# Kernel optimization log

Measured on AMD Instinct MI355X. Metric: run time of the kernel, lower is better.

## Reference

```python
import jax, jax.numpy as jnp
import numpy as np

N_NODES = 100000
N_EDGES = 1600000
HIDDEN = 128
LEAKY_SLOPE = 0.01  # torch F.leaky_relu default


def setup_inputs() -> dict:
    key = jax.random.key(0)
    k1, k2, k3, k4 = jax.random.split(key, 4)
    x = jax.random.normal(k1, (N_NODES, HIDDEN), dtype=jnp.float32)
    edge_index = jax.random.randint(k2, (2, N_EDGES), 0, N_NODES, dtype=jnp.int64)
    # nn.Linear(hidden, 1, bias=False) weights, stored as [hidden] vectors
    w_i = jax.random.normal(k3, (HIDDEN,), dtype=jnp.float32) * (1.0 / np.sqrt(HIDDEN))
    w_j = jax.random.normal(k4, (HIDDEN,), dtype=jnp.float32) * (1.0 / np.sqrt(HIDDEN))
    return {"x": x, "edge_index": edge_index, "w_i": w_i, "w_j": w_j}


def _segment_softmax(e, seg, num_segments):
    # numerically stable softmax over variable-length groups keyed by seg
    seg_max = jax.ops.segment_max(e, seg, num_segments=num_segments)
    seg_max = jnp.where(jnp.isfinite(seg_max), seg_max, 0.0)  # empty segments
    e_exp = jnp.exp(e - seg_max[seg])
    denom = jax.ops.segment_sum(e_exp, seg, num_segments=num_segments)
    return e_exp / denom[seg]


def reference(x, edge_index, w_i, w_j):
    n = x.shape[0]
    idx_j = edge_index[0]  # edge_index_j (softmax groups)
    idx_i = edge_index[1]  # edge_index_i (aggregation destinations)
    # per-node attention logits, gathered per edge
    ei_all = x @ w_i  # [N]
    ej_all = x @ w_j  # [N]
    e = ei_all[idx_i] + ej_all[idx_j]  # [E]
    e = jnp.where(e > 0, e, LEAKY_SLOPE * e)  # leaky_relu
    alpha = _segment_softmax(e.astype(jnp.float32), idx_j, n)  # [E]
    # spmm(edge_index[[1,0]], alpha, N, N, x): out[idx_i] += alpha * x[idx_j]
    msgs = alpha[:, None] * x[idx_j]  # [E, hidden]
    out = jax.ops.segment_sum(msgs, idx_i, num_segments=n)
    return jax.nn.relu(out)
```

## Files before the change

kernel.cpp:

```cpp
#include <hip/hip_runtime.h>

#define N_HID 128
#define LEAKY 0.01f
#define EPB   4096
#define SCB   1024

__device__ inline ushort f2bf_rne(float f) {
    unsigned u = __float_as_uint(f);
    u += 0x7fffu + ((u >> 16) & 1u);
    return (ushort)(u >> 16);
}

__device__ inline int load_idx(const void* eidx, long long pos, int is64) {
    if (is64) return (int)((const long long*)eidx)[pos];
    return ((const int*)eidx)[pos];
}

__global__ void detect_dtype_k(const void* __restrict__ eidx, long long n_i64,
                               int* __restrict__ flag) {
    __shared__ int nonzero_hi;
    if (threadIdx.x == 0) nonzero_hi = 0;
    __syncthreads();
    const long long* p = (const long long*)eidx;
    long long samples = n_i64 < 4096 ? n_i64 : 4096;
    int bad = 0;
    for (long long k = threadIdx.x; k < samples; k += blockDim.x) {
        if ((p[k] >> 32) != 0) bad = 1;
    }
    if (bad) atomicOr(&nonzero_hi, 1);
    __syncthreads();
    if (threadIdx.x == 0) *flag = nonzero_hi ? 0 : 1;
}

__global__ __launch_bounds__(256) void node_logits_k(
        const float* __restrict__ x, const float* __restrict__ w_i,
        const float* __restrict__ w_j, float* __restrict__ ei_all,
        float* __restrict__ ej_all, ushort* __restrict__ xb, int n) {
    int wave = (int)((blockIdx.x * (long long)blockDim.x + threadIdx.x) >> 6);
    int lane = threadIdx.x & 63;
    if (wave >= n) return;
    const float2* xr = (const float2*)(x + (long long)wave * N_HID);
    float2 v  = xr[lane];
    float2 wi = ((const float2*)w_i)[lane];
    float2 wj = ((const float2*)w_j)[lane];
    if (xb) {
        unsigned packed = (unsigned)f2bf_rne(v.x) | ((unsigned)f2bf_rne(v.y) << 16);
        ((unsigned*)(xb + (long long)wave * N_HID))[lane] = packed;
    }
    float si = v.x * wi.x + v.y * wi.y;
    float sj = v.x * wj.x + v.y * wj.y;
    #pragma unroll
    for (int off = 32; off >= 1; off >>= 1) {
        si += __shfl_xor(si, off);
        sj += __shfl_xor(sj, off);
    }
    if (lane == 0) {
        ei_all[wave] = si;
        ej_all[wave] = sj;
    }
}

__global__ __launch_bounds__(256) void hist_k(
        const void* __restrict__ eidx, const int* __restrict__ flag,
        unsigned* __restrict__ tabI, unsigned* __restrict__ tabJ,
        long long E, int nblkA, int NB) {
    __shared__ unsigned hi[512], hj[512];
    for (int b = threadIdx.x; b < NB; b += 256) { hi[b] = 0; hj[b] = 0; }
    __syncthreads();
    int is64 = *flag;
    long long k0 = (long long)blockIdx.x * EPB;
    #pragma unroll 4
    for (int m = 0; m < EPB / 256; ++m) {
        long long k = k0 + m * 256 + threadIdx.x;
        if (k < E) {
            int j = load_idx(eidx, k, is64);
            int i = load_idx(eidx, E + k, is64);
            atomicAdd(&hi[i >> 8], 1u);
            atomicAdd(&hj[j >> 8], 1u);
        }
    }
    __syncthreads();
    for (int b = threadIdx.x; b < NB; b += 256) {
        tabI[(size_t)b * nblkA + blockIdx.x] = hi[b];
        tabJ[(size_t)b * nblkA + blockIdx.x] = hj[b];
    }
}

__global__ __launch_bounds__(SCB) void scanT1_k(unsigned* __restrict__ a,
                                                unsigned* __restrict__ bs, int nt) {
    __shared__ unsigned tmp[SCB];
    int gid = blockIdx.x * SCB + threadIdx.x;
    unsigned v = (gid < nt) ? a[gid] : 0;
    tmp[threadIdx.x] = v;
    __syncthreads();
    for (int off = 1; off < SCB; off <<= 1) {
        unsigned t = (threadIdx.x >= off) ? tmp[threadIdx.x - off] : 0;
        __syncthreads();
        tmp[threadIdx.x] += t;
        __syncthreads();
    }
    if (gid < nt) a[gid] = tmp[threadIdx.x] - v;
    if (threadIdx.x == SCB - 1) bs[blockIdx.x] = tmp[threadIdx.x];
}

__global__ __launch_bounds__(SCB) void scanT2_k(unsigned* __restrict__ bs, int nb) {
    __shared__ unsigned tmp[SCB];
    unsigned v = (threadIdx.x < nb) ? bs[threadIdx.x] : 0;
    tmp[threadIdx.x] = v;
    __syncthreads();
    for (int off = 1; off < SCB; off <<= 1) {
        unsigned t = (threadIdx.x >= off) ? tmp[threadIdx.x - off] : 0;
        __syncthreads();
        tmp[threadIdx.x] += t;
        __syncthreads();
    }
    if (threadIdx.x < nb) bs[threadIdx.x] = tmp[threadIdx.x] - v;
}

__global__ __launch_bounds__(SCB) void scanT3_k(unsigned* __restrict__ a,
                                                const unsigned* __restrict__ bs,
                                                int nt) {
    int gid = blockIdx.x * SCB + threadIdx.x;
    if (gid < nt) a[gid] += bs[gid / SCB];
}

__global__ __launch_bounds__(256) void scatter2_k(
        const void* __restrict__ eidx, const int* __restrict__ flag,
        const unsigned* __restrict__ tabI, const unsigned* __restrict__ tabJ,
        unsigned* __restrict__ srecI, unsigned* __restrict__ srecJ,
        long long E, int nblkA, int NB) {
    __shared__ unsigned ci[512], cj[512];
    unsigned Eu = (unsigned)E;
    for (int b = threadIdx.x; b < NB; b += 256) {
        ci[b] = tabI[(size_t)b * nblkA + blockIdx.x];
        cj[b] = tabJ[(size_t)b * nblkA + blockIdx.x] - Eu;
    }
    __syncthreads();
    int is64 = *flag;
    long long k0 = (long long)blockIdx.x * EPB;
    #pragma unroll 4
    for (int m = 0; m < EPB / 256; ++m) {
        long long k = k0 + m * 256 + threadIdx.x;
        if (k < E) {
            int j = load_idx(eidx, k, is64);
            int i = load_idx(eidx, E + k, is64);
            unsigned pI = atomicAdd(&ci[i >> 8], 1u);
            srecI[pI] = ((unsigned)(i & 255) << 17) | (unsigned)j;
            unsigned pJ = atomicAdd(&cj[j >> 8], 1u);
            srecJ[pJ] = ((unsigned)(j & 255) << 17) | (unsigned)i;
        }
    }
}

__global__ __launch_bounds__(256) void finalizeJ_k(
        const unsigned* __restrict__ srecJ, const unsigned* __restrict__ tabJ,
        const float* __restrict__ ei_all, const float* __restrict__ ej_all,
        float* __restrict__ denom, int n, long long E, int nblkA, int NB) {
    int b = blockIdx.x;
    int tid = threadIdx.x;
    unsigned Eu = (unsigned)E;
    int base = (int)(tabJ[(size_t)b * nblkA] - Eu);
    int end  = (b + 1 < NB) ? (int)(tabJ[(size_t)(b + 1) * nblkA] - Eu) : (int)E;

    __shared__ float ejl[256];
    __shared__ float dsum[256];
    int g = b * 256 + tid;
    ejl[tid]  = (g < n) ? ej_all[g] : 0.f;
    dsum[tid] = 0.f;
    __syncthreads();

    for (int t = base + tid; t < end; t += 256) {
        unsigned r = srecJ[t];
        int jl = (int)(r >> 17);
        int i  = (int)(r & 0x1FFFFu);
        float e = ei_all[i] + ejl[jl];
        e = e > 0.f ? e : LEAKY * e;
        atomicAdd(&dsum[jl], __expf(e));
    }
    __syncthreads();
    if (g < n) denom[g] = dsum[tid];
}

__global__ __launch_bounds__(256) void finalizeI_k(
        const unsigned* __restrict__ srecI, const unsigned* __restrict__ tabI,
        const float* __restrict__ ei_all, const float* __restrict__ ej_all,
        const float* __restrict__ denom, int* __restrict__ start,
        unsigned* __restrict__ pje, int n, long long E, int nblkA, int NB) {
    int b = blockIdx.x;
    int tid = threadIdx.x;
    int base = (int)tabI[(size_t)b * nblkA];
    int end  = (b + 1 < NB) ? (int)tabI[(size_t)(b + 1) * nblkA] : (int)E;

    __shared__ int cnt[256];
    __shared__ int off[256];
    __shared__ float eil[256];
    int g = b * 256 + tid;
    cnt[tid] = 0;
    eil[tid] = (g < n) ? ei_all[g] : 0.f;
    __syncthreads();

    for (int t = base + tid; t < end; t += 256)
        atomicAdd(&cnt[srecI[t] >> 17], 1);
    __syncthreads();

    int v = cnt[tid];
    off[tid] = v;
    __syncthreads();
    for (int s = 1; s < 256; s <<= 1) {
        int t2 = (tid >= s) ? off[tid - s] : 0;
        __syncthreads();
        off[tid] += t2;
        __syncthreads();
    }
    int excl = off[tid] - v;
    if (g < n) start[g] = base + excl;
    if (b == NB - 1 && tid == 0) start[n] = (int)E;

    cnt[tid] = excl;
    __syncthreads();

    for (int t = base + tid; t < end; t += 256) {
        unsigned r = srecI[t];
        int il = (int)(r >> 17);
        int j  = (int)(r & 0x1FFFFu);
        float e = eil[il] + ej_all[j];
        e = e > 0.f ? e : LEAKY * e;
        float alpha = __expf(e) / denom[j];
        unsigned aq = __float2uint_rn(alpha * 32768.f);
        if (aq > 32767u) aq = 32767u;
        int slot = base + atomicAdd(&cnt[il], 1);
        pje[slot] = ((unsigned)j << 15) | aq;
    }
}

__global__ __launch_bounds__(256) void gather_bf16_k(
        const int* __restrict__ start, const unsigned* __restrict__ pje,
        const ushort* __restrict__ xb, float* __restrict__ out, int n) {
    int wave = (int)((blockIdx.x * (long long)blockDim.x + threadIdx.x) >> 6);
    int lane = threadIdx.x & 63;
    if (wave >= n) return;
    int s = start[wave];
    int e_end = start[wave + 1];
    int sub = lane >> 4;
    int col = lane & 15;

    float a0 = 0.f, a1 = 0.f, a2 = 0.f, a3 = 0.f;
    float a4 = 0.f, a5 = 0.f, a6 = 0.f, a7 = 0.f;
    for (int e = s; e < e_end; e += 8) {
        int ee0 = e + sub;
        int ee1 = e + 4 + sub;
        unsigned cur0 = (ee0 < e_end) ? pje[ee0] : 0u;
        unsigned cur1 = (ee1 < e_end) ? pje[ee1] : 0u;
        float af0 = (float)(cur0 & 0x7FFFu) * (1.f / 32768.f);
        float af1 = (float)(cur1 & 0x7FFFu) * (1.f / 32768.f);
        uint4 u0 = ((const uint4*)(xb + (size_t)(cur0 >> 15) * N_HID))[col];
        uint4 u1 = ((const uint4*)(xb + (size_t)(cur1 >> 15) * N_HID))[col];
        a0 += af0 * __uint_as_float(u0.x << 16);
        a1 += af0 * __uint_as_float(u0.x & 0xffff0000u);
        a2 += af0 * __uint_as_float(u0.y << 16);
        a3 += af0 * __uint_as_float(u0.y & 0xffff0000u);
        a4 += af0 * __uint_as_float(u0.z << 16);
        a5 += af0 * __uint_as_float(u0.z & 0xffff0000u);
        a6 += af0 * __uint_as_float(u0.w << 16);
        a7 += af0 * __uint_as_float(u0.w & 0xffff0000u);
        a0 += af1 * __uint_as_float(u1.x << 16);
        a1 += af1 * __uint_as_float(u1.x & 0xffff0000u);
        a2 += af1 * __uint_as_float(u1.y << 16);
        a3 += af1 * __uint_as_float(u1.y & 0xffff0000u);
        a4 += af1 * __uint_as_float(u1.z << 16);
        a5 += af1 * __uint_as_float(u1.z & 0xffff0000u);
        a6 += af1 * __uint_as_float(u1.w << 16);
        a7 += af1 * __uint_as_float(u1.w & 0xffff0000u);
    }
    a0 += __shfl_xor(a0, 16); a1 += __shfl_xor(a1, 16);
    a2 += __shfl_xor(a2, 16); a3 += __shfl_xor(a3, 16);
    a4 += __shfl_xor(a4, 16); a5 += __shfl_xor(a5, 16);
    a6 += __shfl_xor(a6, 16); a7 += __shfl_xor(a7, 16);
    a0 += __shfl_xor(a0, 32); a1 += __shfl_xor(a1, 32);
    a2 += __shfl_xor(a2, 32); a3 += __shfl_xor(a3, 32);
    a4 += __shfl_xor(a4, 32); a5 += __shfl_xor(a5, 32);
    a6 += __shfl_xor(a6, 32); a7 += __shfl_xor(a7, 32);

    float4* orow = (float4*)(out + (size_t)wave * N_HID);
    if (sub == 0) {
        float4 r;
        r.x = fmaxf(a0, 0.f); r.y = fmaxf(a1, 0.f);
        r.z = fmaxf(a2, 0.f); r.w = fmaxf(a3, 0.f);
        orow[col * 2] = r;
    } else if (sub == 1) {
        float4 r;
        r.x = fmaxf(a4, 0.f); r.y = fmaxf(a5, 0.f);
        r.z = fmaxf(a6, 0.f); r.w = fmaxf(a7, 0.f);
        orow[col * 2 + 1] = r;
    }
}

__global__ __launch_bounds__(256) void gather_f32_k(
        const int* __restrict__ start, const unsigned* __restrict__ pje,
        const float* __restrict__ x, float* __restrict__ out, int n) {
    int wave = (int)((blockIdx.x * (long long)blockDim.x + threadIdx.x) >> 6);
    int lane = threadIdx.x & 63;
    if (wave >= n) return;
    int s = start[wave];
    int e_end = start[wave + 1];
    float ax = 0.f, ay = 0.f;
    unsigned ja = 0;
    if (s < e_end) ja = pje[s];
    for (int e = s; e < e_end; ++e) {
        unsigned cur = ja;
        if (e + 1 < e_end) ja = pje[e + 1];
        float a = (float)(cur & 0x7FFFu) * (1.f / 32768.f);
        float2 v = ((const float2*)(x + (long long)(cur >> 15) * N_HID))[lane];
        ax += a * v.x;
        ay += a * v.y;
    }
    float2 r;
    r.x = fmaxf(ax, 0.f);
    r.y = fmaxf(ay, 0.f);
    ((float2*)(out + (long long)wave * N_HID))[lane] = r;
}

extern "C" void kernel_launch(void* const* d_in, const int* in_sizes, int n_in,
                              void* d_out, int out_size, void* d_ws,
                              size_t ws_size, hipStream_t stream) {
    const float* x   = (const float*)d_in[0];
    const void*  eix = d_in[1];
    const float* w_i = (const float*)d_in[2];
    const float* w_j = (const float*)d_in[3];
    float* out = (float*)d_out;

    int n = in_sizes[0] / N_HID;
    long long E = in_sizes[1] / 2;

    int nblkA = (int)((E + EPB - 1) / EPB);
    int NB    = (n + 255) / 256;
    int NT    = NB * nblkA;
    int NT2   = 2 * NT;
    int nb1   = (NT2 + SCB - 1) / SCB;

    char* p = (char*)d_ws;
    float* ei_all = (float*)p;               p += (size_t)n * 4;
    float* ej_all = (float*)p;               p += (size_t)n * 4;
    float* denom  = (float*)p;               p += (size_t)n * 4;
    int*   start  = (int*)p;                 p += ((size_t)(n + 1) * 4 + 15) & ~15ull;
    unsigned* tab = (unsigned*)p;            p += ((size_t)NT2 * 4 + 15) & ~15ull;
    unsigned* tabI = tab;
    unsigned* tabJ = tab + NT;
    unsigned* bs1 = (unsigned*)p;            p += (size_t)SCB * 4;
    int*   flag   = (int*)p;                 p += 16;
    unsigned* srecI = (unsigned*)p;          p += (size_t)E * 4;
    unsigned* pje   = (unsigned*)p;          p += (size_t)E * 4;
    unsigned* srecJ = pje;
    ushort* xb    = (ushort*)p;              p += (size_t)n * N_HID * 2;
    int wsBig = ((size_t)(p - (char*)d_ws) <= ws_size);
    if (!wsBig) xb = nullptr;

    detect_dtype_k<<<1, 256, 0, stream>>>(eix, E * 2, flag);

    long long t1 = (long long)n * 64;
    node_logits_k<<<(unsigned)((t1 + 255) / 256), 256, 0, stream>>>(
        x, w_i, w_j, ei_all, ej_all, xb, n);

    hist_k<<<nblkA, 256, 0, stream>>>(eix, flag, tabI, tabJ, E, nblkA, NB);

    scanT1_k<<<nb1, SCB, 0, stream>>>(tab, bs1, NT2);
    scanT2_k<<<1, SCB, 0, stream>>>(bs1, nb1);
    scanT3_k<<<nb1, SCB, 0, stream>>>(tab, bs1, NT2);

    scatter2_k<<<nblkA, 256, 0, stream>>>(eix, flag, tabI, tabJ, srecI, srecJ,
                                          E, nblkA, NB);

    finalizeJ_k<<<NB, 256, 0, stream>>>(srecJ, tabJ, ei_all, ej_all, denom,
                                        n, E, nblkA, NB);

    finalizeI_k<<<NB, 256, 0, stream>>>(srecI, tabI, ei_all, ej_all, denom,
                                        start, pje, n, E, nblkA, NB);

    long long t4 = (long long)n * 64;
    if (wsBig) {
        gather_bf16_k<<<(unsigned)((t4 + 255) / 256), 256, 0, stream>>>(
            start, pje, xb, out, n);
    } else {
        gather_f32_k<<<(unsigned)((t4 + 255) / 256), 256, 0, stream>>>(
            start, pje, x, out, n);
    }
}
```

Before: 202.9 us.

## Fold scan block offsets into consumers, widen finalize blocks, pack logit/denominator

Drops the third scan pass by having scatter and both finalize kernels add the per-chunk scan offset on the fly when reading the table. The finalize kernels now launch with 512 threads over each 256-node bucket to expose more parallelism. The j-side logit and softmax denominator are packed into one float2 so the I-side gather does one load per edge. EPB is also halved, which doubles the number of histogram blocks and the size of the prefix table.

```diff
diff --git a/kernel.cpp b/kernel.cpp
--- a/kernel.cpp
+++ b/kernel.cpp
@@ -2,8 +2,9 @@
 
 #define N_HID 128
 #define LEAKY 0.01f
-#define EPB   4096
+#define EPB   2048
 #define SCB   1024
+#define TABV(g) (tab[g] + bs1[(g) >> 10])
 
 __device__ inline ushort f2bf_rne(float f) {
     unsigned u = __float_as_uint(f);
@@ -117,23 +118,18 @@
     if (threadIdx.x < nb) bs[threadIdx.x] = tmp[threadIdx.x] - v;
 }
 
-__global__ __launch_bounds__(SCB) void scanT3_k(unsigned* __restrict__ a,
-                                                const unsigned* __restrict__ bs,
-                                                int nt) {
-    int gid = blockIdx.x * SCB + threadIdx.x;
-    if (gid < nt) a[gid] += bs[gid / SCB];
-}
-
 __global__ __launch_bounds__(256) void scatter2_k(
         const void* __restrict__ eidx, const int* __restrict__ flag,
-        const unsigned* __restrict__ tabI, const unsigned* __restrict__ tabJ,
+        const unsigned* __restrict__ tab, const unsigned* __restrict__ bs1,
         unsigned* __restrict__ srecI, unsigned* __restrict__ srecJ,
-        long long E, int nblkA, int NB) {
+        long long E, int nblkA, int NB, int NT) {
     __shared__ unsigned ci[512], cj[512];
     unsigned Eu = (unsigned)E;
     for (int b = threadIdx.x; b < NB; b += 256) {
-        ci[b] = tabI[(size_t)b * nblkA + blockIdx.x];
-        cj[b] = tabJ[(size_t)b * nblkA + blockIdx.x] - Eu;
+        size_t gI = (size_t)b * nblkA + blockIdx.x;
+        size_t gJ = (size_t)NT + gI;
+        ci[b] = TABV(gI);
+        cj[b] = TABV(gJ) - Eu;
     }
     __syncthreads();
     int is64 = *flag;
@@ -152,24 +148,28 @@
     }
 }
 
-__global__ __launch_bounds__(256) void finalizeJ_k(
-        const unsigned* __restrict__ srecJ, const unsigned* __restrict__ tabJ,
-        const float* __restrict__ ei_all, const float* __restrict__ ej_all,
-        float* __restrict__ denom, int n, long long E, int nblkA, int NB) {
+__global__ __launch_bounds__(512) void finalizeJ_k(
+        const unsigned* __restrict__ srecJ, const unsigned* __restrict__ tab,
+        const unsigned* __restrict__ bs1, const float* __restrict__ ei_all,
+        const float* __restrict__ ej_all, float2* __restrict__ ejd,
+        int n, long long E, int nblkA, int NB, int NT) {
     int b = blockIdx.x;
     int tid = threadIdx.x;
     unsigned Eu = (unsigned)E;
-    int base = (int)(tabJ[(size_t)b * nblkA] - Eu);
-    int end  = (b + 1 < NB) ? (int)(tabJ[(size_t)(b + 1) * nblkA] - Eu) : (int)E;
+    size_t gJ0 = (size_t)NT + (size_t)b * nblkA;
+    int base = (int)(TABV(gJ0) - Eu);
+    int end  = (b + 1 < NB) ? (int)(TABV(gJ0 + nblkA) - Eu) : (int)E;
 
     __shared__ float ejl[256];
     __shared__ float dsum[256];
     int g = b * 256 + tid;
-    ejl[tid]  = (g < n) ? ej_all[g] : 0.f;
-    dsum[tid] = 0.f;
-    __syncthreads();
-
-    for (int t = base + tid; t < end; t += 256) {
+    if (tid < 256) {
+        ejl[tid]  = (g < n) ? ej_all[g] : 0.f;
+        dsum[tid] = 0.f;
+    }
+    __syncthreads();
+
+    for (int t = base + tid; t < end; t += 512) {
         unsigned r = srecJ[t];
         int jl = (int)(r >> 17);
         int i  = (int)(r & 0x1FFFFu);
@@ -178,54 +178,66 @@
         atomicAdd(&dsum[jl], __expf(e));
     }
     __syncthreads();
-    if (g < n) denom[g] = dsum[tid];
-}
-
-__global__ __launch_bounds__(256) void finalizeI_k(
-        const unsigned* __restrict__ srecI, const unsigned* __restrict__ tabI,
-        const float* __restrict__ ei_all, const float* __restrict__ ej_all,
-        const float* __restrict__ denom, int* __restrict__ start,
-        unsigned* __restrict__ pje, int n, long long E, int nblkA, int NB) {
+    if (tid < 256 && g < n) {
+        float2 r2;
+        r2.x = ejl[tid];
+        r2.y = dsum[tid];
+        ejd[g] = r2;
+    }
+}
+
+__global__ __launch_bounds__(512) void finalizeI_k(
+        const unsigned* __restrict__ srecI, const unsigned* __restrict__ tab,
+        const unsigned* __restrict__ bs1, const float* __restrict__ ei_all,
+        const float2* __restrict__ ejd, int* __restrict__ start,
+        unsigned* __restrict__ pje, int n, long long E, int nblkA, int NB,
+        int NT) {
     int b = blockIdx.x;
     int tid = threadIdx.x;
-    int base = (int)tabI[(size_t)b * nblkA];
-    int end  = (b + 1 < NB) ? (int)tabI[(size_t)(b + 1) * nblkA] : (int)E;
+    size_t gI0 = (size_t)b * nblkA;
+    int base = (int)TABV(gI0);
+    int end  = (b + 1 < NB) ? (int)TABV(gI0 + nblkA) : (int)E;
 
     __shared__ int cnt[256];
     __shared__ int off[256];
     __shared__ float eil[256];
     int g = b * 256 + tid;
-    cnt[tid] = 0;
-    eil[tid] = (g < n) ? ei_all[g] : 0.f;
-    __syncthreads();
-
-    for (int t = base + tid; t < end; t += 256)
+    if (tid < 256) {
+        cnt[tid] = 0;
+        eil[tid] = (g < n) ? ei_all[g] : 0.f;
+    }
+    __syncthreads();
+
+    for (int t = base + tid; t < end; t += 512)
         atomicAdd(&cnt[srecI[t] >> 17], 1);
     __syncthreads();
 
-    int v = cnt[tid];
-    off[tid] = v;
+    int v = 0;
+    if (tid < 256) { v = cnt[tid]; off[tid] = v; }
     __syncthreads();
     for (int s = 1; s < 256; s <<= 1) {
-        int t2 = (tid >= s) ? off[tid - s] : 0;
-        __syncthreads();
-        off[tid] += t2;
-        __syncthreads();
-    }
-    int excl = off[tid] - v;
-    if (g < n) start[g] = base + excl;
+        int t2 = 0;
+        if (tid < 256 && tid >= s) t2 = off[tid - s];
+        __syncthreads();
+        if (tid < 256) off[tid] += t2;
+        __syncthreads();
+    }
+    if (tid < 256) {
+        int excl = off[tid] - v;
+        if (g < n) start[g] = base + excl;
+        cnt[tid] = excl;
+    }
     if (b == NB - 1 && tid == 0) start[n] = (int)E;
-
-    cnt[tid] = excl;
-    __syncthreads();
-
-    for (int t = base + tid; t < end; t += 256) {
+    __syncthreads();
+
+    for (int t = base + tid; t < end; t += 512) {
         unsigned r = srecI[t];
         int il = (int)(r >> 17);
         int j  = (int)(r & 0x1FFFFu);
-        float e = eil[il] + ej_all[j];
+        float2 ed = ejd[j];
+        float e = eil[il] + ed.x;
         e = e > 0.f ? e : LEAKY * e;
-        float alpha = __expf(e) / denom[j];
+        float alpha = __expf(e) / ed.y;
         unsigned aq = __float2uint_rn(alpha * 32768.f);
         if (aq > 32767u) aq = 32767u;
         int slot = base + atomicAdd(&cnt[il], 1);
@@ -341,7 +353,7 @@
     char* p = (char*)d_ws;
     float* ei_all = (float*)p;               p += (size_t)n * 4;
     float* ej_all = (float*)p;               p += (size_t)n * 4;
-    float* denom  = (float*)p;               p += (size_t)n * 4;
+    float2* ejd   = (float2*)p;              p += (size_t)n * 8;
     int*   start  = (int*)p;                 p += ((size_t)(n + 1) * 4 + 15) & ~15ull;
     unsigned* tab = (unsigned*)p;            p += ((size_t)NT2 * 4 + 15) & ~15ull;
     unsigned* tabI = tab;
@@ -365,16 +377,15 @@
 
     scanT1_k<<<nb1, SCB, 0, stream>>>(tab, bs1, NT2);
     scanT2_k<<<1, SCB, 0, stream>>>(bs1, nb1);
-    scanT3_k<<<nb1, SCB, 0, stream>>>(tab, bs1, NT2);
-
-    scatter2_k<<<nblkA, 256, 0, stream>>>(eix, flag, tabI, tabJ, srecI, srecJ,
-                                          E, nblkA, NB);
-
-    finalizeJ_k<<<NB, 256, 0, stream>>>(srecJ, tabJ, ei_all, ej_all, denom,
-                                        n, E, nblkA, NB);
-
-    finalizeI_k<<<NB, 256, 0, stream>>>(srecI, tabI, ei_all, ej_all, denom,
-                                        start, pje, n, E, nblkA, NB);
+
+    scatter2_k<<<nblkA, 256, 0, stream>>>(eix, flag, tab, bs1, srecI, srecJ,
+                                          E, nblkA, NB, NT);
+
+    finalizeJ_k<<<NB, 512, 0, stream>>>(srecJ, tab, bs1, ei_all, ej_all, ejd,
+                                        n, E, nblkA, NB, NT);
+
+    finalizeI_k<<<NB, 512, 0, stream>>>(srecI, tab, bs1, ei_all, ejd,
+                                        start, pje, n, E, nblkA, NB, NT);
 
     long long t4 = (long long)n * 64;
     if (wsBig) {
```

New measurement: 201.9 us. No clear change (-0.5%).
